# Optimization experiments

Measured on AMD Instinct MI355X. Metric: run time of the kernel, lower is better.

## Reference

```python
import jax, jax.numpy as jnp
import numpy as np

H = 1024


def _gru_dir(xg, h0, w_hh, b_hh, reverse):
    # xg: (L, G, 3H) precomputed input-gate projections; h0: (G, H)
    def step(h, xt):
        hg = h @ w_hh.T + b_hh
        xr, xz, xn = jnp.split(xt, 3, axis=-1)
        hr, hz, hn = jnp.split(hg, 3, axis=-1)
        r = jax.nn.sigmoid(xr + hr)
        z = jax.nn.sigmoid(xz + hz)
        n = jnp.tanh(xn + r * hn)
        h_new = (1.0 - z) * n + z * h
        return h_new, h_new
    _, hs = jax.lax.scan(step, h0, xg, reverse=reverse)
    return hs  # (L, G, H), time-ordered (scan reverse keeps original order)


def setup_inputs() -> dict:
    key = jax.random.key(0)
    ks = jax.random.split(key, 12)
    N, G, L = 16384, 256, 128
    s = 1.0 / np.sqrt(H)
    inp = {
        "h_atom": jax.random.normal(ks[0], (N, H), dtype=jnp.float32),
        "batch": jnp.sort(jax.random.randint(ks[1], (N,), 0, G)),
        "bias": jax.random.uniform(ks[2], (H,), jnp.float32, -s, s),
        "w_ih_f": jax.random.uniform(ks[3], (3 * H, H), jnp.float32, -s, s),
        "w_hh_f": jax.random.uniform(ks[4], (3 * H, H), jnp.float32, -s, s),
        "b_ih_f": jax.random.uniform(ks[5], (3 * H,), jnp.float32, -s, s),
        "b_hh_f": jax.random.uniform(ks[6], (3 * H,), jnp.float32, -s, s),
        "w_ih_b": jax.random.uniform(ks[7], (3 * H, H), jnp.float32, -s, s),
        "w_hh_b": jax.random.uniform(ks[8], (3 * H, H), jnp.float32, -s, s),
        "b_ih_b": jax.random.uniform(ks[9], (3 * H,), jnp.float32, -s, s),
        "b_hh_b": jax.random.uniform(ks[10], (3 * H,), jnp.float32, -s, s),
        "num_graphs": G,
        "pad_len": L,
    }
    return inp


def reference(h_atom, bias, w_ih_f, w_hh_f, b_ih_f, b_hh_f,
              w_ih_b, w_hh_b, b_ih_b, b_hh_b, batch, num_graphs, pad_len):
    N = h_atom.shape[0]
    G, L = num_graphs, pad_len
    message = jax.nn.relu(h_atom + bias)  # (N, H)

    # per-graph counts / positions (batch is sorted by graph id)
    counts = jax.ops.segment_sum(jnp.ones((N,), jnp.int32), batch, num_segments=G)
    start = jnp.cumsum(counts) - counts
    pos = jnp.arange(N) - start[batch]  # position of each atom within its graph

    # pad ragged atoms -> (G, L, H); padded slots stay zero (matches torch)
    msgs = jnp.zeros((G, L, H), h_atom.dtype).at[batch, pos].set(message)

    # segment-max hidden init, shared by both directions
    h0 = jax.ops.segment_max(h_atom, batch, num_segments=G)  # (G, H)
    h0 = jnp.where(counts[:, None] > 0, h0, 0.0)

    # precompute input-gate projections, time-major
    xg_f = jnp.einsum('glh,kh->lgk', msgs, w_ih_f) + b_ih_f  # (L, G, 3H)
    xg_b = jnp.einsum('glh,kh->lgk', msgs, w_ih_b) + b_ih_b

    hs_f = _gru_dir(xg_f, h0, w_hh_f, b_hh_f, reverse=False)  # (L, G, H)
    hs_b = _gru_dir(xg_b, h0, w_hh_b, b_hh_b, reverse=True)   # (L, G, H)

    h_messages = jnp.concatenate([hs_f, hs_b], axis=-1).transpose(1, 0, 2)  # (G, L, 2H)

    # unpad back to (N, 2H)
    return h_messages[batch, pos]
```

## Files before the change

### kernel.cpp

```cpp
#include <hip/hip_runtime.h>
#include <stdint.h>

#define H 1024
#define G_ 256
#define LPAD 128

typedef float  floatx4 __attribute__((ext_vector_type(4)));
typedef short  shortx8 __attribute__((ext_vector_type(8)));

#define MFMA(a, b, c) __builtin_amdgcn_mfma_f32_16x16x32_bf16((a), (b), (c), 0, 0, 0)

__device__ __forceinline__ uint16_t f2bf(float f) {
  union { float f; uint32_t i; } v; v.f = f;
  uint32_t r = (v.i + 0x7FFFu + ((v.i >> 16) & 1u)) >> 16;
  return (uint16_t)r;
}
__device__ __forceinline__ float bf2f(uint16_t u) {
  union { uint32_t i; float f; } v; v.i = ((uint32_t)u) << 16; return v.f;
}
__device__ __forceinline__ float sigmoid_(float x) { return 1.f / (1.f + __expf(-x)); }
__device__ __forceinline__ float tanh_(float x) {
  float ax = fabsf(x);
  float e = __expf(2.f * ax);
  float t = 1.f - 2.f / (e + 1.f);
  return x >= 0.f ? t : -t;
}

__global__ void k_f2b(const float* __restrict__ src, uint16_t* __restrict__ dst) {
  size_t i = ((size_t)blockIdx.x * blockDim.x + threadIdx.x) * 8;
  float4 a = *(const float4*)(src + i);
  float4 b = *(const float4*)(src + i + 4);
  uint16_t o[8] = {f2bf(a.x), f2bf(a.y), f2bf(a.z), f2bf(a.w),
                   f2bf(b.x), f2bf(b.y), f2bf(b.z), f2bf(b.w)};
  uint4 ov; __builtin_memcpy(&ov, o, 16);
  *(uint4*)(dst + i) = ov;
}

__global__ void k_setup(const int* __restrict__ batch, int N, int* __restrict__ start) {
  int g = threadIdx.x;
  if (g > G_) return;
  int lo = 0, hi = N;
  while (lo < hi) { int mid = (lo + hi) >> 1; if (batch[mid] < g) lo = mid + 1; else hi = mid; }
  start[g] = lo;
}

__global__ void k_msg(const float* __restrict__ h_atom, const float* __restrict__ bias,
                      uint16_t* __restrict__ msg) {
  int row = blockIdx.x, t = threadIdx.x;
  size_t off = (size_t)row * H + t * 8;
  float4 h0 = *(const float4*)(h_atom + off);
  float4 h1 = *(const float4*)(h_atom + off + 4);
  float4 b0 = *(const float4*)(bias + t * 8);
  float4 b1 = *(const float4*)(bias + t * 8 + 4);
  float v[8] = {h0.x + b0.x, h0.y + b0.y, h0.z + b0.z, h0.w + b0.w,
                h1.x + b1.x, h1.y + b1.y, h1.z + b1.z, h1.w + b1.w};
  uint16_t o[8];
#pragma unroll
  for (int i = 0; i < 8; i++) o[i] = f2bf(v[i] > 0.f ? v[i] : 0.f);
  uint4 ov; __builtin_memcpy(&ov, o, 16);
  *(uint4*)(msg + off) = ov;
}

__global__ void k_h0(const float* __restrict__ h_atom, const int* __restrict__ start,
                     float* __restrict__ hf32, uint16_t* __restrict__ hbf) {
  int g = blockIdx.x, t = threadIdx.x;
  int s = start[g], e = start[g + 1];
  float m[4] = {-INFINITY, -INFINITY, -INFINITY, -INFINITY};
  const float* base = h_atom + t * 4;
  for (int a = s; a < e; a++) {
    float4 v = *(const float4*)(base + (size_t)a * H);
    m[0] = fmaxf(m[0], v.x); m[1] = fmaxf(m[1], v.y);
    m[2] = fmaxf(m[2], v.z); m[3] = fmaxf(m[3], v.w);
  }
  if (s == e) { m[0] = m[1] = m[2] = m[3] = 0.f; }
#pragma unroll
  for (int i = 0; i < 4; i++) {
    int c = t * 4 + i;
    float mv = m[i];
    uint16_t bv = f2bf(mv);
    hf32[(size_t)0 * G_ * H + (size_t)g * H + c] = mv;
    hf32[(size_t)2 * G_ * H + (size_t)g * H + c] = mv;
    hbf [(size_t)0 * G_ * H + (size_t)g * H + c] = bv;
    hbf [(size_t)2 * G_ * H + (size_t)g * H + c] = bv;
  }
}

__global__ __launch_bounds__(256) void k_gemm_xg(
    const uint16_t* __restrict__ A, const uint16_t* __restrict__ Wf,
    const uint16_t* __restrict__ Wb, uint16_t* __restrict__ C, int N) {
  __shared__ __align__(16) uint16_t As[128 * 64];
  __shared__ __align__(16) uint16_t Bs[128 * 64];
  int bn = blockIdx.x, bm = blockIdx.y;
  const uint16_t* B = (bn < 24) ? Wf : Wb;
  int brow = (bn < 24 ? bn : bn - 24) * 128;
  int tid = threadIdx.x, wid = tid >> 6, lane = tid & 63;
  int wm = wid >> 1, wn = wid & 1;
  floatx4 acc[4][4];
#pragma unroll
  for (int mi = 0; mi < 4; mi++)
#pragma unroll
    for (int ni = 0; ni < 4; ni++) acc[mi][ni] = (floatx4){0.f, 0.f, 0.f, 0.f};
  int arow = bm * 128;
  for (int kb = 0; kb < H; kb += 64) {
    uint4 av[4], bv[4];
#pragma unroll
    for (int p = 0; p < 4; p++) {
      int c = p * 256 + tid;
      av[p] = *(const uint4*)(A + (size_t)(arow + (c >> 3)) * H + kb + (c & 7) * 8);
      bv[p] = *(const uint4*)(B + (size_t)(brow + (c >> 3)) * H + kb + (c & 7) * 8);
    }
    __syncthreads();
#pragma unroll
    for (int p = 0; p < 4; p++) {
      int c = p * 256 + tid;
      *(uint4*)(As + (size_t)c * 8) = av[p];
      *(uint4*)(Bs + (size_t)c * 8) = bv[p];
    }
    __syncthreads();
#pragma unroll
    for (int ks = 0; ks < 2; ks++) {
      const uint16_t* ab = As + ((wm * 64 + (lane & 15)) * 64 + ks * 32 + (lane >> 4) * 8);
      const uint16_t* bb = Bs + ((wn * 64 + (lane & 15)) * 64 + ks * 32 + (lane >> 4) * 8);
      shortx8 af[4], bfr[4];
#pragma unroll
      for (int i = 0; i < 4; i++) {
        af[i]  = *(const shortx8*)(ab + i * 16 * 64);
        bfr[i] = *(const shortx8*)(bb + i * 16 * 64);
      }
#pragma unroll
      for (int mi = 0; mi < 4; mi++)
#pragma unroll
        for (int ni = 0; ni < 4; ni++)
          acc[mi][ni] = MFMA(af[mi], bfr[ni], acc[mi][ni]);
    }
  }
  int colb = bn * 128 + wn * 64 + (lane & 15);
  int rowb = bm * 128 + wm * 64 + (lane >> 4) * 4;
#pragma unroll
  for (int mi = 0; mi < 4; mi++)
#pragma unroll
    for (int ni = 0; ni < 4; ni++) {
      size_t base = (size_t)(rowb + mi * 16) * 6144 + colb + ni * 16;
#pragma unroll
      for (int r = 0; r < 4; r++) C[base + (size_t)r * 6144] = f2bf(acc[mi][ni][r]);
    }
}

__global__ __launch_bounds__(256) void k_step(
    int l, const uint16_t* __restrict__ xg,
    const uint16_t* __restrict__ whf, const uint16_t* __restrict__ whb,
    const float* __restrict__ bihf, const float* __restrict__ bhhf,
    const float* __restrict__ bihb, const float* __restrict__ bhhb,
    float* __restrict__ hf32, uint16_t* __restrict__ hbf,
    const int* __restrict__ start, float* __restrict__ out) {
  __shared__ __align__(16) uint16_t As[64 * 64];
  __shared__ __align__(16) uint16_t Bs[96 * 64];
  __shared__ float HG[64 * 97];
  int b = blockIdx.x;
  int e = b & 7, hi = b >> 3;
  int d = e >> 2, jm = e & 3;
  int jc = (hi & 7) * 4 + jm;
  int g0 = (hi >> 3) * 64;
  int cur = l & 1;
  const uint16_t* W = d ? whb : whf;
  const uint16_t* hsrc = hbf + (size_t)(d * 2 + cur) * G_ * H;
  int tid = threadIdx.x, wid = tid >> 6, lane = tid & 63;
  int wm = wid >> 1, wn = wid & 1;
  floatx4 acc[2][3];
#pragma unroll
  for (int mi = 0; mi < 2; mi++)
#pragma unroll
    for (int ni = 0; ni < 3; ni++) acc[mi][ni] = (floatx4){0.f, 0.f, 0.f, 0.f};

  for (int kb = 0; kb < H; kb += 64) {
    uint4 av[2], bv[3];
#pragma unroll
    for (int p = 0; p < 2; p++) {
      int c = p * 256 + tid;
      av[p] = *(const uint4*)(hsrc + (size_t)(g0 + (c >> 3)) * H + kb + (c & 7) * 8);
    }
#pragma unroll
    for (int p = 0; p < 3; p++) {
      int c = p * 256 + tid;
      int row = c >> 3;
      int wrow = (row >> 5) * H + jc * 32 + (row & 31);
      bv[p] = *(const uint4*)(W + (size_t)wrow * H + kb + (c & 7) * 8);
    }
    __syncthreads();
#pragma unroll
    for (int p = 0; p < 2; p++) *(uint4*)(As + (size_t)(p * 256 + tid) * 8) = av[p];
#pragma unroll
    for (int p = 0; p < 3; p++) *(uint4*)(Bs + (size_t)(p * 256 + tid) * 8) = bv[p];
    __syncthreads();
#pragma unroll
    for (int ks = 0; ks < 2; ks++) {
      const uint16_t* ab = As + ((wm * 32 + (lane & 15)) * 64 + ks * 32 + (lane >> 4) * 8);
      const uint16_t* bb = Bs + ((wn * 48 + (lane & 15)) * 64 + ks * 32 + (lane >> 4) * 8);
      shortx8 a0 = *(const shortx8*)ab;
      shortx8 a1 = *(const shortx8*)(ab + 16 * 64);
#pragma unroll
      for (int ni = 0; ni < 3; ni++) {
        shortx8 bvf = *(const shortx8*)(bb + ni * 16 * 64);
        acc[0][ni] = MFMA(a0, bvf, acc[0][ni]);
        acc[1][ni] = MFMA(a1, bvf, acc[1][ni]);
      }
    }
  }
  __syncthreads();
#pragma unroll
  for (int mi = 0; mi < 2; mi++)
#pragma unroll
    for (int ni = 0; ni < 3; ni++) {
      int row0 = wm * 32 + mi * 16 + (lane >> 4) * 4;
      int col = wn * 48 + ni * 16 + (lane & 15);
#pragma unroll
      for (int r = 0; r < 4; r++) HG[(row0 + r) * 97 + col] = acc[mi][ni][r];
    }
  __syncthreads();

  int base = tid * 8;
  int gl = base >> 5, j0 = base & 31;
  int g = g0 + gl;
  int s = start[g], cnt = start[g + 1] - s;
  int t = d ? (LPAD - 1 - l) : l;
  bool active = (t < cnt);
  int col0 = jc * 32 + j0;
  const float* bih = d ? bihb : bihf;
  const float* bhh = d ? bhhb : bhhf;
  const uint16_t* xp = xg + (size_t)(s + t) * 6144 + (size_t)d * 3072;
  const float* h_old = hf32 + ((size_t)(d * 2 + cur) * G_ + g) * H + col0;
  float* h_new32 = hf32 + ((size_t)(d * 2 + (cur ^ 1)) * G_ + g) * H + col0;
  uint16_t* h_newb = hbf + ((size_t)(d * 2 + (cur ^ 1)) * G_ + g) * H + col0;
  float* op = out + (size_t)(s + t) * 2048 + (size_t)d * H + col0;
#pragma unroll
  for (int i = 0; i < 8; i++) {
    int c = col0 + i;
    float hr = HG[gl * 97 + j0 + i];
    float hz = HG[gl * 97 + 32 + j0 + i];
    float hn = HG[gl * 97 + 64 + j0 + i];
    float xr = 0.f, xz = 0.f, xn = 0.f;
    if (active) { xr = bf2f(xp[c]); xz = bf2f(xp[H + c]); xn = bf2f(xp[2 * H + c]); }
    float r = sigmoid_(xr + bih[c] + hr + bhh[c]);
    float z = sigmoid_(xz + bih[H + c] + hz + bhh[H + c]);
    float n = tanh_(xn + bih[2 * H + c] + r * (hn + bhh[2 * H + c]));
    float hv = h_old[i];
    float hnew = (1.f - z) * n + z * hv;
    h_new32[i] = hnew;
    h_newb[i] = f2bf(hnew);
    if (active) op[i] = hnew;
  }
}

extern "C" void kernel_launch(void* const* d_in, const int* in_sizes, int n_in,
                              void* d_out, int out_size, void* d_ws, size_t ws_size,
                              hipStream_t stream) {
  const float* h_atom = (const float*)d_in[0];
  const int*   batch  = (const int*)d_in[1];
  const float* bias   = (const float*)d_in[2];
  const float* w_ih_f = (const float*)d_in[3];
  const float* w_hh_f = (const float*)d_in[4];
  const float* b_ih_f = (const float*)d_in[5];
  const float* b_hh_f = (const float*)d_in[6];
  const float* w_ih_b = (const float*)d_in[7];
  const float* w_hh_b = (const float*)d_in[8];
  const float* b_ih_b = (const float*)d_in[9];
  const float* b_hh_b = (const float*)d_in[10];
  int N = in_sizes[0] / H;
  float* out = (float*)d_out;

  const size_t W3 = (size_t)3 * H * H;
  char* ws = (char*)d_ws;
  uint16_t* msg  = (uint16_t*)ws;
  uint16_t* xg   = (uint16_t*)(ws + (size_t)N * H * 2);
  char* p = ws + (size_t)N * H * 2 + (size_t)N * 6144 * 2;
  uint16_t* wihf = (uint16_t*)p; p += W3 * 2;
  uint16_t* wihb = (uint16_t*)p; p += W3 * 2;
  uint16_t* whhf = (uint16_t*)p; p += W3 * 2;
  uint16_t* whhb = (uint16_t*)p; p += W3 * 2;
  float*    hf32 = (float*)p;    p += (size_t)4 * G_ * H * 4;
  uint16_t* hbf  = (uint16_t*)p; p += (size_t)4 * G_ * H * 2;
  int*      start = (int*)p;

  int wgrid = (int)(W3 / (256 * 8));
  k_f2b<<<wgrid, 256, 0, stream>>>(w_ih_f, wihf);
  k_f2b<<<wgrid, 256, 0, stream>>>(w_ih_b, wihb);
  k_f2b<<<wgrid, 256, 0, stream>>>(w_hh_f, whhf);
  k_f2b<<<wgrid, 256, 0, stream>>>(w_hh_b, whhb);
  k_setup<<<1, 512, 0, stream>>>(batch, N, start);
  k_msg<<<N, 128, 0, stream>>>(h_atom, bias, msg);
  k_h0<<<G_, 256, 0, stream>>>(h_atom, start, hf32, hbf);
  k_gemm_xg<<<dim3(48, N / 128), 256, 0, stream>>>(msg, wihf, wihb, xg, N);
  for (int l = 0; l < LPAD; l++)
    k_step<<<256, 256, 0, stream>>>(l, xg, whhf, whhb, b_ih_f, b_hh_f,
                                    b_ih_b, b_hh_b, hf32, hbf, start, out);
}
```

Before: 8.251 ms.

## Replace per-step GRU launches with persistent kernel using grid-wide flag barrier

Replaces the 128 per-timestep k_step launches with one persistent kernel of 256 blocks. Each block keeps its slice of the recurrent weights resident in LDS and its fp32 hidden state in registers, and all blocks sync each step through a spin-wait on per-block atomic flags. This removes per-step launch overhead and the repeated weight reloads from global memory. The input-projection GEMM also gets padded LDS rows and a coalesced store staged through shared memory. The cost is that the grid barrier depends on all 256 blocks being co-resident, and every block polls 256 flags each step.

```diff
diff --git a/kernel.cpp b/kernel.cpp
--- a/kernel.cpp
+++ b/kernel.cpp
@@ -4,6 +4,7 @@
 #define H 1024
 #define G_ 256
 #define LPAD 128
+#define GH (G_ * H)
 
 typedef float  floatx4 __attribute__((ext_vector_type(4)));
 typedef short  shortx8 __attribute__((ext_vector_type(8)));
@@ -36,8 +37,10 @@
   *(uint4*)(dst + i) = ov;
 }
 
-__global__ void k_setup(const int* __restrict__ batch, int N, int* __restrict__ start) {
+__global__ void k_setup(const int* __restrict__ batch, int N, int* __restrict__ start,
+                        int* __restrict__ flags) {
   int g = threadIdx.x;
+  if (g < 256) flags[g] = 0;
   if (g > G_) return;
   int lo = 0, hi = N;
   while (lo < hi) { int mid = (lo + hi) >> 1; if (batch[mid] < g) lo = mid + 1; else hi = mid; }
@@ -78,18 +81,19 @@
     int c = t * 4 + i;
     float mv = m[i];
     uint16_t bv = f2bf(mv);
-    hf32[(size_t)0 * G_ * H + (size_t)g * H + c] = mv;
-    hf32[(size_t)2 * G_ * H + (size_t)g * H + c] = mv;
-    hbf [(size_t)0 * G_ * H + (size_t)g * H + c] = bv;
-    hbf [(size_t)2 * G_ * H + (size_t)g * H + c] = bv;
+    hf32[(size_t)0 * GH + (size_t)g * H + c] = mv;
+    hf32[(size_t)2 * GH + (size_t)g * H + c] = mv;
+    hbf [(size_t)0 * GH + (size_t)g * H + c] = bv;
+    hbf [(size_t)2 * GH + (size_t)g * H + c] = bv;
   }
 }
 
 __global__ __launch_bounds__(256) void k_gemm_xg(
     const uint16_t* __restrict__ A, const uint16_t* __restrict__ Wf,
     const uint16_t* __restrict__ Wb, uint16_t* __restrict__ C, int N) {
-  __shared__ __align__(16) uint16_t As[128 * 64];
-  __shared__ __align__(16) uint16_t Bs[128 * 64];
+  __shared__ __align__(16) uint16_t smem[2 * 128 * 72];
+  uint16_t* As = smem;
+  uint16_t* Bs = smem + 128 * 72;
   int bn = blockIdx.x, bm = blockIdx.y;
   const uint16_t* B = (bn < 24) ? Wf : Wb;
   int brow = (bn < 24 ? bn : bn - 24) * 128;
@@ -113,19 +117,19 @@
 #pragma unroll
     for (int p = 0; p < 4; p++) {
       int c = p * 256 + tid;
-      *(uint4*)(As + (size_t)c * 8) = av[p];
-      *(uint4*)(Bs + (size_t)c * 8) = bv[p];
+      *(uint4*)(As + (c >> 3) * 72 + (c & 7) * 8) = av[p];
+      *(uint4*)(Bs + (c >> 3) * 72 + (c & 7) * 8) = bv[p];
     }
     __syncthreads();
 #pragma unroll
     for (int ks = 0; ks < 2; ks++) {
-      const uint16_t* ab = As + ((wm * 64 + (lane & 15)) * 64 + ks * 32 + (lane >> 4) * 8);
-      const uint16_t* bb = Bs + ((wn * 64 + (lane & 15)) * 64 + ks * 32 + (lane >> 4) * 8);
+      const uint16_t* ab = As + (wm * 64 + (lane & 15)) * 72 + ks * 32 + (lane >> 4) * 8;
+      const uint16_t* bb = Bs + (wn * 64 + (lane & 15)) * 72 + ks * 32 + (lane >> 4) * 8;
       shortx8 af[4], bfr[4];
 #pragma unroll
       for (int i = 0; i < 4; i++) {
-        af[i]  = *(const shortx8*)(ab + i * 16 * 64);
-        bfr[i] = *(const shortx8*)(bb + i * 16 * 64);
+        af[i]  = *(const shortx8*)(ab + i * 16 * 72);
+        bfr[i] = *(const shortx8*)(bb + i * 16 * 72);
       }
 #pragma unroll
       for (int mi = 0; mi < 4; mi++)
@@ -134,120 +138,151 @@
           acc[mi][ni] = MFMA(af[mi], bfr[ni], acc[mi][ni]);
     }
   }
-  int colb = bn * 128 + wn * 64 + (lane & 15);
-  int rowb = bm * 128 + wm * 64 + (lane >> 4) * 4;
+  __syncthreads();
+  uint16_t* Cs = smem;
 #pragma unroll
   for (int mi = 0; mi < 4; mi++)
 #pragma unroll
     for (int ni = 0; ni < 4; ni++) {
-      size_t base = (size_t)(rowb + mi * 16) * 6144 + colb + ni * 16;
-#pragma unroll
-      for (int r = 0; r < 4; r++) C[base + (size_t)r * 6144] = f2bf(acc[mi][ni][r]);
-    }
-}
-
-__global__ __launch_bounds__(256) void k_step(
-    int l, const uint16_t* __restrict__ xg,
-    const uint16_t* __restrict__ whf, const uint16_t* __restrict__ whb,
+      int row0 = wm * 64 + mi * 16 + (lane >> 4) * 4;
+      int col  = wn * 64 + ni * 16 + (lane & 15);
+#pragma unroll
+      for (int r = 0; r < 4; r++) Cs[(row0 + r) * 136 + col] = f2bf(acc[mi][ni][r]);
+    }
+  __syncthreads();
+#pragma unroll
+  for (int p = 0; p < 8; p++) {
+    int flat = p * 256 + tid;
+    int row = flat >> 4, ch = flat & 15;
+    *(uint4*)(C + (size_t)(arow + row) * 6144 + bn * 128 + ch * 8) =
+        *(const uint4*)(Cs + row * 136 + ch * 8);
+  }
+}
+
+__global__ __launch_bounds__(256, 1) void k_persist(
+    const uint16_t* __restrict__ xg,
+    const uint16_t* __restrict__ whhf, const uint16_t* __restrict__ whhb,
     const float* __restrict__ bihf, const float* __restrict__ bhhf,
     const float* __restrict__ bihb, const float* __restrict__ bhhb,
-    float* __restrict__ hf32, uint16_t* __restrict__ hbf,
-    const int* __restrict__ start, float* __restrict__ out) {
-  __shared__ __align__(16) uint16_t As[64 * 64];
-  __shared__ __align__(16) uint16_t Bs[96 * 64];
-  __shared__ float HG[64 * 97];
+    const float* __restrict__ hf32, uint16_t* __restrict__ hbf,
+    const int* __restrict__ start, float* __restrict__ out,
+    int* __restrict__ flags) {
+  __shared__ __align__(16) uint16_t Ws[48 * 1032];
+  __shared__ __align__(16) uint16_t As[2 * 128 * 72];
   int b = blockIdx.x;
-  int e = b & 7, hi = b >> 3;
-  int d = e >> 2, jm = e & 3;
-  int jc = (hi & 7) * 4 + jm;
-  int g0 = (hi >> 3) * 64;
-  int cur = l & 1;
-  const uint16_t* W = d ? whb : whf;
-  const uint16_t* hsrc = hbf + (size_t)(d * 2 + cur) * G_ * H;
+  int jc = b & 63, d = (b >> 6) & 1, gh = b >> 7;
   int tid = threadIdx.x, wid = tid >> 6, lane = tid & 63;
-  int wm = wid >> 1, wn = wid & 1;
-  floatx4 acc[2][3];
-#pragma unroll
-  for (int mi = 0; mi < 2; mi++)
-#pragma unroll
-    for (int ni = 0; ni < 3; ni++) acc[mi][ni] = (floatx4){0.f, 0.f, 0.f, 0.f};
-
-  for (int kb = 0; kb < H; kb += 64) {
-    uint4 av[2], bv[3];
-#pragma unroll
-    for (int p = 0; p < 2; p++) {
-      int c = p * 256 + tid;
-      av[p] = *(const uint4*)(hsrc + (size_t)(g0 + (c >> 3)) * H + kb + (c & 7) * 8);
-    }
-#pragma unroll
-    for (int p = 0; p < 3; p++) {
-      int c = p * 256 + tid;
-      int row = c >> 3;
-      int wrow = (row >> 5) * H + jc * 32 + (row & 31);
-      bv[p] = *(const uint4*)(W + (size_t)wrow * H + kb + (c & 7) * 8);
-    }
-    __syncthreads();
-#pragma unroll
-    for (int p = 0; p < 2; p++) *(uint4*)(As + (size_t)(p * 256 + tid) * 8) = av[p];
-#pragma unroll
-    for (int p = 0; p < 3; p++) *(uint4*)(Bs + (size_t)(p * 256 + tid) * 8) = bv[p];
-    __syncthreads();
-#pragma unroll
-    for (int ks = 0; ks < 2; ks++) {
-      const uint16_t* ab = As + ((wm * 32 + (lane & 15)) * 64 + ks * 32 + (lane >> 4) * 8);
-      const uint16_t* bb = Bs + ((wn * 48 + (lane & 15)) * 64 + ks * 32 + (lane >> 4) * 8);
-      shortx8 a0 = *(const shortx8*)ab;
-      shortx8 a1 = *(const shortx8*)(ab + 16 * 64);
-#pragma unroll
-      for (int ni = 0; ni < 3; ni++) {
-        shortx8 bvf = *(const shortx8*)(bb + ni * 16 * 64);
-        acc[0][ni] = MFMA(a0, bvf, acc[0][ni]);
-        acc[1][ni] = MFMA(a1, bvf, acc[1][ni]);
-      }
-    }
-  }
-  __syncthreads();
-#pragma unroll
-  for (int mi = 0; mi < 2; mi++)
-#pragma unroll
-    for (int ni = 0; ni < 3; ni++) {
-      int row0 = wm * 32 + mi * 16 + (lane >> 4) * 4;
-      int col = wn * 48 + ni * 16 + (lane & 15);
-#pragma unroll
-      for (int r = 0; r < 4; r++) HG[(row0 + r) * 97 + col] = acc[mi][ni][r];
-    }
-  __syncthreads();
-
-  int base = tid * 8;
-  int gl = base >> 5, j0 = base & 31;
-  int g = g0 + gl;
-  int s = start[g], cnt = start[g + 1] - s;
-  int t = d ? (LPAD - 1 - l) : l;
-  bool active = (t < cnt);
-  int col0 = jc * 32 + j0;
+  const uint16_t* W = d ? whhb : whhf;
   const float* bih = d ? bihb : bihf;
   const float* bhh = d ? bhhb : bhhf;
-  const uint16_t* xp = xg + (size_t)(s + t) * 6144 + (size_t)d * 3072;
-  const float* h_old = hf32 + ((size_t)(d * 2 + cur) * G_ + g) * H + col0;
-  float* h_new32 = hf32 + ((size_t)(d * 2 + (cur ^ 1)) * G_ + g) * H + col0;
-  uint16_t* h_newb = hbf + ((size_t)(d * 2 + (cur ^ 1)) * G_ + g) * H + col0;
-  float* op = out + (size_t)(s + t) * 2048 + (size_t)d * H + col0;
-#pragma unroll
-  for (int i = 0; i < 8; i++) {
-    int c = col0 + i;
-    float hr = HG[gl * 97 + j0 + i];
-    float hz = HG[gl * 97 + 32 + j0 + i];
-    float hn = HG[gl * 97 + 64 + j0 + i];
-    float xr = 0.f, xz = 0.f, xn = 0.f;
-    if (active) { xr = bf2f(xp[c]); xz = bf2f(xp[H + c]); xn = bf2f(xp[2 * H + c]); }
-    float r = sigmoid_(xr + bih[c] + hr + bhh[c]);
-    float z = sigmoid_(xz + bih[H + c] + hz + bhh[H + c]);
-    float n = tanh_(xn + bih[2 * H + c] + r * (hn + bhh[2 * H + c]));
-    float hv = h_old[i];
-    float hnew = (1.f - z) * n + z * hv;
-    h_new32[i] = hnew;
-    h_newb[i] = f2bf(hnew);
-    if (active) op[i] = hnew;
+  int col16 = lane & 15;
+  int col = jc * 16 + col16;
+
+#pragma unroll
+  for (int p = 0; p < 24; p++) {
+    int flat = p * 256 + tid;
+    int row = flat >> 7, ch = flat & 127;
+    *(uint4*)(Ws + row * 1032 + ch * 8) =
+        *(const uint4*)(W + (size_t)((row >> 4) * H + jc * 16 + (row & 15)) * H + ch * 8);
+  }
+
+  float hreg[8], bihv[3], bhhv[3];
+  int sg[8], cntg[8], gar[8];
+#pragma unroll
+  for (int q = 0; q < 3; q++) { bihv[q] = bih[q * H + col]; bhhv[q] = bhh[q * H + col]; }
+#pragma unroll
+  for (int m = 0; m < 2; m++)
+#pragma unroll
+    for (int r = 0; r < 4; r++) {
+      int sl = m * 4 + r;
+      int grow = wid * 32 + m * 16 + (lane >> 4) * 4 + r;
+      int g = gh * 128 + grow;
+      gar[sl] = g;
+      sg[sl] = start[g];
+      cntg[sl] = start[g + 1] - sg[sl];
+      hreg[sl] = hf32[(size_t)(d * 2) * GH + (size_t)g * H + col];
+    }
+  __syncthreads();
+
+  const int abase = wid * 32 + (lane & 15);
+  const int koff = (lane >> 4) * 8;
+
+  for (int t = 0; t < LPAD; t++) {
+    int cur = t & 1;
+    const uint16_t* hsrc = hbf + (size_t)(d * 2 + cur) * GH + (size_t)gh * 128 * H;
+    size_t ndst = (size_t)(d * 2 + (cur ^ 1)) * GH;
+    floatx4 acc[2][3];
+#pragma unroll
+    for (int m = 0; m < 2; m++)
+#pragma unroll
+      for (int n = 0; n < 3; n++) acc[m][n] = (floatx4){0.f, 0.f, 0.f, 0.f};
+
+    uint4 areg[4];
+#pragma unroll
+    for (int p = 0; p < 4; p++) {
+      int c = p * 256 + tid;
+      areg[p] = *(const uint4*)(hsrc + (size_t)(c >> 3) * H + (c & 7) * 8);
+    }
+    for (int kb = 0; kb < 16; kb++) {
+      uint16_t* Ab = As + (kb & 1) * (128 * 72);
+#pragma unroll
+      for (int p = 0; p < 4; p++) {
+        int c = p * 256 + tid;
+        *(uint4*)(Ab + (c >> 3) * 72 + (c & 7) * 8) = areg[p];
+      }
+      __syncthreads();
+      if (kb < 15) {
+#pragma unroll
+        for (int p = 0; p < 4; p++) {
+          int c = p * 256 + tid;
+          areg[p] = *(const uint4*)(hsrc + (size_t)(c >> 3) * H + (kb + 1) * 64 + (c & 7) * 8);
+        }
+      }
+      const uint16_t* ab = Ab + abase * 72 + koff;
+      const uint16_t* wb = Ws + (lane & 15) * 1032 + kb * 64 + koff;
+#pragma unroll
+      for (int ks = 0; ks < 2; ks++) {
+        shortx8 a0 = *(const shortx8*)(ab + ks * 32);
+        shortx8 a1 = *(const shortx8*)(ab + 16 * 72 + ks * 32);
+#pragma unroll
+        for (int n = 0; n < 3; n++) {
+          shortx8 bv = *(const shortx8*)(wb + n * 16 * 1032 + ks * 32);
+          acc[0][n] = MFMA(a0, bv, acc[0][n]);
+          acc[1][n] = MFMA(a1, bv, acc[1][n]);
+        }
+      }
+    }
+
+#pragma unroll
+    for (int m = 0; m < 2; m++)
+#pragma unroll
+      for (int r = 0; r < 4; r++) {
+        int sl = m * 4 + r;
+        int t_g = d ? (LPAD - 1 - t) : t;
+        bool act = t_g < cntg[sl];
+        float xr = 0.f, xz = 0.f, xn = 0.f;
+        if (act) {
+          const uint16_t* xp = xg + (size_t)(sg[sl] + t_g) * 6144 + d * 3072 + col;
+          xr = bf2f(xp[0]); xz = bf2f(xp[H]); xn = bf2f(xp[2 * H]);
+        }
+        float rv = sigmoid_(xr + bihv[0] + acc[m][0][r] + bhhv[0]);
+        float zv = sigmoid_(xz + bihv[1] + acc[m][1][r] + bhhv[1]);
+        float nv = tanh_(xn + bihv[2] + rv * (acc[m][2][r] + bhhv[2]));
+        float hnew = (1.f - zv) * nv + zv * hreg[sl];
+        hreg[sl] = hnew;
+        hbf[ndst + (size_t)gar[sl] * H + col] = f2bf(hnew);
+        if (act) out[(size_t)(sg[sl] + t_g) * 2048 + d * H + col] = hnew;
+      }
+
+    if (t < LPAD - 1) {
+      __threadfence();
+      __syncthreads();
+      if (tid == 0)
+        __hip_atomic_store(&flags[b], t + 1, __ATOMIC_RELEASE, __HIP_MEMORY_SCOPE_AGENT);
+      while (__hip_atomic_load(&flags[tid], __ATOMIC_ACQUIRE, __HIP_MEMORY_SCOPE_AGENT) < t + 1)
+        __builtin_amdgcn_s_sleep(2);
+      __syncthreads();
+    }
   }
 }
 
@@ -277,20 +312,20 @@
   uint16_t* wihb = (uint16_t*)p; p += W3 * 2;
   uint16_t* whhf = (uint16_t*)p; p += W3 * 2;
   uint16_t* whhb = (uint16_t*)p; p += W3 * 2;
-  float*    hf32 = (float*)p;    p += (size_t)4 * G_ * H * 4;
-  uint16_t* hbf  = (uint16_t*)p; p += (size_t)4 * G_ * H * 2;
-  int*      start = (int*)p;
+  float*    hf32 = (float*)p;    p += (size_t)4 * GH * 4;
+  uint16_t* hbf  = (uint16_t*)p; p += (size_t)4 * GH * 2;
+  int*      start = (int*)p;     p += 1024;
+  int*      flags = (int*)p;
 
   int wgrid = (int)(W3 / (256 * 8));
   k_f2b<<<wgrid, 256, 0, stream>>>(w_ih_f, wihf);
   k_f2b<<<wgrid, 256, 0, stream>>>(w_ih_b, wihb);
   k_f2b<<<wgrid, 256, 0, stream>>>(w_hh_f, whhf);
   k_f2b<<<wgrid, 256, 0, stream>>>(w_hh_b, whhb);
-  k_setup<<<1, 512, 0, stream>>>(batch, N, start);
+  k_setup<<<1, 512, 0, stream>>>(batch, N, start, flags);
   k_msg<<<N, 128, 0, stream>>>(h_atom, bias, msg);
   k_h0<<<G_, 256, 0, stream>>>(h_atom, start, hf32, hbf);
   k_gemm_xg<<<dim3(48, N / 128), 256, 0, stream>>>(msg, wihf, wihb, xg, N);
-  for (int l = 0; l < LPAD; l++)
-    k_step<<<256, 256, 0, stream>>>(l, xg, whhf, whhb, b_ih_f, b_hh_f,
-                                    b_ih_b, b_hh_b, hf32, hbf, start, out);
-}
+  k_persist<<<256, 256, 0, stream>>>(xg, whhf, whhb, b_ih_f, b_hh_f, b_ih_b, b_hh_b,
+                                     hf32, hbf, start, out, flags);
+}
```

Result: slower. 9.917 ms (+20.2%).
